# Kernel optimization log

Hardware: AMD Instinct MI355X
Metric: run time of the kernel (lower is better)

The kernel has to match this reference:

```python
import jax, jax.numpy as jnp
import numpy as np

N = 100000   # nodes
E = 1600000  # edges
NEG_SLOPE = 0.2
EPS = 1e-16


def _layer_norm(x, g, b):
    mu = jnp.mean(x, axis=-1, keepdims=True)
    var = jnp.mean((x - mu) ** 2, axis=-1, keepdims=True)
    return (x - mu) * jax.lax.rsqrt(var + 1e-5) * g + b


def _gat_layer(x, W, att_s, att_d, bias, src, dst, heads, C):
    n = x.shape[0]
    h = (x @ W.T).reshape(n, heads, C)            # [N,H,C]
    sa = jnp.sum(h * att_s, axis=-1)              # [N,H]
    da = jnp.sum(h * att_d, axis=-1)              # [N,H]
    logits = jax.nn.leaky_relu(sa[src] + da[dst], NEG_SLOPE)  # [E,H]
    m = jax.ops.segment_max(logits, dst, num_segments=n)      # [N,H]
    m = jnp.where(jnp.isfinite(m), m, 0.0)
    w = jnp.exp(logits - m[dst])                  # [E,H]
    denom = jax.ops.segment_sum(w, dst, num_segments=n)       # [N,H]
    msg = h[src] * w[:, :, None]                  # [E,H,C]
    agg = jax.ops.segment_sum(msg, dst, num_segments=n)       # [N,H,C]
    agg = agg / jnp.maximum(denom, EPS)[:, :, None]
    out = (agg + h).reshape(n, heads * C) + bias  # residual + bias
    return out


def setup_inputs() -> dict:
    key = jax.random.key(0)
    ks = jax.random.split(key, 16)
    s = 0.05
    inp = {
        "x": jax.random.normal(ks[0], (N, 128), jnp.float32),
        "edge_src": jax.random.randint(ks[1], (E,), 0, N, jnp.int32),
        "edge_dst": jax.random.randint(ks[2], (E,), 0, N, jnp.int32),
        # layer 1: in 128 -> heads=2, C=32 (out width 64)
        "W1": jax.random.normal(ks[3], (64, 128), jnp.float32) * s,
        "as1": jax.random.normal(ks[4], (2, 32), jnp.float32) * s,
        "ad1": jax.random.normal(ks[5], (2, 32), jnp.float32) * s,
        "b1": jnp.zeros((64,), jnp.float32),
        # layer 2: 64 -> heads=2, C=32
        "W2": jax.random.normal(ks[6], (64, 64), jnp.float32) * s,
        "as2": jax.random.normal(ks[7], (2, 32), jnp.float32) * s,
        "ad2": jax.random.normal(ks[8], (2, 32), jnp.float32) * s,
        "b2": jnp.zeros((64,), jnp.float32),
        # layer 3 (last): 64 -> heads=1, C=32
        "W3": jax.random.normal(ks[9], (32, 64), jnp.float32) * s,
        "as3": jax.random.normal(ks[10], (1, 32), jnp.float32) * s,
        "ad3": jax.random.normal(ks[11], (1, 32), jnp.float32) * s,
        "b3": jnp.zeros((32,), jnp.float32),
        "gamma1": jnp.ones((64,), jnp.float32),
        "beta1": jnp.zeros((64,), jnp.float32),
        "gamma2": jnp.ones((64,), jnp.float32),
        "beta2": jnp.zeros((64,), jnp.float32),
    }
    return inp


def reference(x, edge_src, edge_dst, W1, as1, ad1, b1, W2, as2, ad2, b2,
              W3, as3, ad3, b3, gamma1, beta1, gamma2, beta2):
    h = _gat_layer(x, W1, as1, ad1, b1, edge_src, edge_dst, 2, 32)
    h = jax.nn.relu(_layer_norm(h, gamma1, beta1))
    h = _gat_layer(h, W2, as2, ad2, b2, edge_src, edge_dst, 2, 32)
    h = jax.nn.relu(_layer_norm(h, gamma2, beta2))
    h = _gat_layer(h, W3, as3, ad3, b3, edge_src, edge_dst, 1, 32)
    return h
```

## Files before the change

kernel.cpp:

```cpp
#include <hip/hip_runtime.h>
#include <hip/hip_fp16.h>

#define LEAKY 0.2f
#define BSH 7
#define BN 128
#define CHUNK 8192
#define NBMAX 1024

__device__ __forceinline__ float leaky(float l) {
  return l >= 0.f ? l : LEAKY * l;
}

typedef _Float16 f16x2 __attribute__((ext_vector_type(2)));

__device__ __forceinline__ float fdot2(unsigned a, unsigned b, float c) {
#if __has_builtin(__builtin_amdgcn_fdot2)
  return __builtin_amdgcn_fdot2(__builtin_bit_cast(f16x2, a),
                                __builtin_bit_cast(f16x2, b), c, false);
#else
  __half2 ha = *(__half2*)&a, hb = *(__half2*)&b;
  float2 fa = __half22float2(ha), fb = __half22float2(hb);
  return fmaf(fa.x, fb.x, fmaf(fa.y, fb.y, c));
#endif
}

__device__ __forceinline__ int packsplat(float w) {
  const __half2 s = __half2half2(__float2half(w));
  return *(const int*)&s;
}
__device__ __forceinline__ __half2 asH2(unsigned u) { return *(__half2*)&u; }

template<int K, int CO, int H, bool IN_F32>
__global__ __launch_bounds__(256, 6)
void gat_gemm3(const void* __restrict__ xin, const float* __restrict__ W,
               const float* __restrict__ atts, const float* __restrict__ attd,
               __half* __restrict__ hh, float* __restrict__ sa, float* __restrict__ da,
               int N) {
  constexpr int CG = CO / 4;
  constexpr int BM = (256 / CG) * 4;
  constexpr int BK = 64;
  constexpr int NK = K / BK;
  constexpr int C = CO / H;
  constexpr int LDW = BK / 2 + 4;

  __shared__ unsigned xs[BM][LDW];
  __shared__ unsigned ws[CO][LDW];

  const int t = (int)threadIdx.x;
  const int cg = t % CG;
  const int ng = t / CG;
  const int n0 = (int)blockIdx.x * BM;

  float acc[4][4] = {};

  for (int kb = 0; kb < NK; ++kb) {
    __syncthreads();
    if constexpr (IN_F32) {
      const float* x = (const float*)xin;
      constexpr int F4R = BK / 4;
      constexpr int TOT = BM * F4R;
      for (int f = t; f < TOT; f += 256) {
        const int r = f / F4R, c = f % F4R;
        int row = n0 + r; row = row < N ? row : N - 1;
        const float4 v = *(const float4*)(x + (size_t)row * K + kb * BK + c * 4);
        const __half2 h0 = __floats2half2_rn(v.x, v.y);
        const __half2 h1 = __floats2half2_rn(v.z, v.w);
        xs[r][c * 2]     = *(const unsigned*)&h0;
        xs[r][c * 2 + 1] = *(const unsigned*)&h1;
      }
    } else {
      const __half* x = (const __half*)xin;
      constexpr int U4R = BK / 8;
      constexpr int TOT = BM * U4R;
      for (int f = t; f < TOT; f += 256) {
        const int r = f / U4R, c = f % U4R;
        int row = n0 + r; row = row < N ? row : N - 1;
        const uint4 v = *(const uint4*)(x + (size_t)row * K + kb * BK + c * 8);
        *(uint4*)&xs[r][c * 4] = v;
      }
    }
    {
      constexpr int F4R = BK / 4;
      constexpr int TOT = CO * F4R;
      for (int f = t; f < TOT; f += 256) {
        const int r = f / F4R, c = f % F4R;
        const float4 v = *(const float4*)(W + (size_t)r * K + kb * BK + c * 4);
        const __half2 h0 = __floats2half2_rn(v.x, v.y);
        const __half2 h1 = __floats2half2_rn(v.z, v.w);
        ws[r][c * 2]     = *(const unsigned*)&h0;
        ws[r][c * 2 + 1] = *(const unsigned*)&h1;
      }
    }
    __syncthreads();
    #pragma unroll
    for (int k = 0; k < BK; k += 8) {
      uint4 xa[4], wb[4];
      #pragma unroll
      for (int i = 0; i < 4; ++i) xa[i] = *(const uint4*)&xs[ng * 4 + i][k / 2];
      #pragma unroll
      for (int j = 0; j < 4; ++j) wb[j] = *(const uint4*)&ws[cg + CG * j][k / 2];
      #pragma unroll
      for (int i = 0; i < 4; ++i) {
        #pragma unroll
        for (int j = 0; j < 4; ++j) {
          acc[i][j] = fdot2(xa[i].x, wb[j].x, acc[i][j]);
          acc[i][j] = fdot2(xa[i].y, wb[j].y, acc[i][j]);
          acc[i][j] = fdot2(xa[i].z, wb[j].z, acc[i][j]);
          acc[i][j] = fdot2(xa[i].w, wb[j].w, acc[i][j]);
        }
      }
    }
  }

  float as_[4], ad_[4];
  #pragma unroll
  for (int j = 0; j < 4; ++j) {
    as_[j] = atts[cg + CG * j];
    ad_[j] = attd[cg + CG * j];
  }
  float ps[4][H] = {}, pd[4][H] = {};
  #pragma unroll
  for (int i = 0; i < 4; ++i) {
    #pragma unroll
    for (int j = 0; j < 4; ++j) {
      const int hd = (CG * j) / C;
      ps[i][hd] = fmaf(acc[i][j], as_[j], ps[i][hd]);
      pd[i][hd] = fmaf(acc[i][j], ad_[j], pd[i][hd]);
    }
  }
  #pragma unroll
  for (int m = 1; m < CG; m <<= 1) {
    #pragma unroll
    for (int i = 0; i < 4; ++i) {
      #pragma unroll
      for (int hd = 0; hd < H; ++hd) {
        ps[i][hd] += __shfl_xor(ps[i][hd], m, 64);
        pd[i][hd] += __shfl_xor(pd[i][hd], m, 64);
      }
    }
  }

  #pragma unroll
  for (int i = 0; i < 4; ++i) {
    const int n = n0 + ng * 4 + i;
    if (n < N) {
      #pragma unroll
      for (int j = 0; j < 4; ++j)
        hh[(size_t)n * CO + cg + CG * j] = __float2half(acc[i][j]);
      if (cg == 0) {
        #pragma unroll
        for (int hd = 0; hd < H; ++hd) {
          sa[n * H + hd] = ps[i][hd];
          da[n * H + hd] = pd[i][hd];
        }
      }
    }
  }
}

__global__ __launch_bounds__(256)
void gat_edge2(const __half* __restrict__ hh,
               const float* __restrict__ sa, const float* __restrict__ da,
               const int* __restrict__ rowp, const int* __restrict__ col,
               const float* __restrict__ bias, const float* __restrict__ gamma,
               const float* __restrict__ beta, __half* __restrict__ out, int N) {
  __shared__ int2 wst[4][4][17][2];
  const int t = (int)threadIdx.x;
  const int lane = t & 63;
  const int wib = t >> 6;
  const int quarter = lane >> 4;
  const int l = lane & 15;
  const int headq = l >> 3;
  const int wgl = (int)((blockIdx.x * blockDim.x + t) >> 6);
  const int n = wgl * 4 + quarter;
  const bool valid = (n < N);
  const int nc = valid ? n : N - 1;
  const int beg = rowp[nc];
  const int end = rowp[nc + 1];
  const float2 dvv = *(const float2*)(da + (size_t)nc * 2);
  const __half2* __restrict__ hhp = (const __half2*)hh;

  const __half2 z = __float2half2_rn(0.f);
  __half2 aL0 = z, aH0 = z, aL1 = z, aH1 = z, aL2 = z, aH2 = z, aL3 = z, aH3 = z;
  __half2 q0 = z, q1 = z, q2 = z, q3 = z;

  for (int b0 = beg; b0 < end; b0 += 16) {
    const int cnt = min(16, end - b0);
    if (l < cnt) {
      const int s = col[b0 + l];
      const float2 p = *(const float2*)(sa + (size_t)s * 2);
      int2 e0; e0.x = s; e0.y = packsplat(__expf(leaky(p.x + dvv.x)));
      int2 e1; e1.x = s; e1.y = packsplat(__expf(leaky(p.y + dvv.y)));
      wst[wib][quarter][l][0] = e0;
      wst[wib][quarter][l][1] = e1;
    }
    int i = 0;
    for (; i + 4 <= cnt; i += 4) {
      const int2 e0 = wst[wib][quarter][i][headq];
      const int2 e1 = wst[wib][quarter][i + 1][headq];
      const int2 e2 = wst[wib][quarter][i + 2][headq];
      const int2 e3 = wst[wib][quarter][i + 3][headq];
      const uint2 h0 = *(const uint2*)(hhp + ((size_t)e0.x << 5) + 2 * l);
      const uint2 h1 = *(const uint2*)(hhp + ((size_t)e1.x << 5) + 2 * l);
      const uint2 h2 = *(const uint2*)(hhp + ((size_t)e2.x << 5) + 2 * l);
      const uint2 h3 = *(const uint2*)(hhp + ((size_t)e3.x << 5) + 2 * l);
      const __half2 w0 = asH2(e0.y), w1 = asH2(e1.y), w2 = asH2(e2.y), w3 = asH2(e3.y);
      q0 = __hadd2(q0, w0); q1 = __hadd2(q1, w1);
      q2 = __hadd2(q2, w2); q3 = __hadd2(q3, w3);
      aL0 = __hfma2(w0, asH2(h0.x), aL0); aH0 = __hfma2(w0, asH2(h0.y), aH0);
      aL1 = __hfma2(w1, asH2(h1.x), aL1); aH1 = __hfma2(w1, asH2(h1.y), aH1);
      aL2 = __hfma2(w2, asH2(h2.x), aL2); aH2 = __hfma2(w2, asH2(h2.y), aH2);
      aL3 = __hfma2(w3, asH2(h3.x), aL3); aH3 = __hfma2(w3, asH2(h3.y), aH3);
    }
    for (; i < cnt; ++i) {
      const int2 e = wst[wib][quarter][i][headq];
      const uint2 hv = *(const uint2*)(hhp + ((size_t)e.x << 5) + 2 * l);
      const __half2 w = asH2(e.y);
      q0 = __hadd2(q0, w);
      aL0 = __hfma2(w, asH2(hv.x), aL0);
      aH0 = __hfma2(w, asH2(hv.y), aH0);
    }
  }

  const float c0 = (__low2float(aL0) + __low2float(aL1)) + (__low2float(aL2) + __low2float(aL3));
  const float c1 = (__high2float(aL0) + __high2float(aL1)) + (__high2float(aL2) + __high2float(aL3));
  const float c2 = (__low2float(aH0) + __low2float(aH1)) + (__low2float(aH2) + __low2float(aH3));
  const float c3 = (__high2float(aH0) + __high2float(aH1)) + (__high2float(aH2) + __high2float(aH3));
  const float qf = (__low2float(q0) + __low2float(q1)) + (__low2float(q2) + __low2float(q3));

  const float inv = 1.f / fmaxf(qf, 1e-16f);
  const uint2 hr = *(const uint2*)(hhp + ((size_t)nc << 5) + 2 * l);
  const float2 r01 = __half22float2(asH2(hr.x));
  const float2 r23 = __half22float2(asH2(hr.y));
  const float4 bi = *(const float4*)(bias + 4 * l);
  float v0 = c0 * inv + r01.x + bi.x;
  float v1 = c1 * inv + r01.y + bi.y;
  float v2 = c2 * inv + r23.x + bi.z;
  float v3 = c3 * inv + r23.y + bi.w;
  {
    float s = (v0 + v1) + (v2 + v3);
    #pragma unroll
    for (int m = 1; m < 16; m <<= 1) s += __shfl_xor(s, m, 64);
    const float mu = s * (1.f / 64.f);
    const float d0 = v0 - mu, d1 = v1 - mu, d2 = v2 - mu, d3 = v3 - mu;
    float vs = (d0 * d0 + d1 * d1) + (d2 * d2 + d3 * d3);
    #pragma unroll
    for (int m = 1; m < 16; m <<= 1) vs += __shfl_xor(vs, m, 64);
    const float rs = rsqrtf(vs * (1.f / 64.f) + 1e-5f);
    const float4 g = *(const float4*)(gamma + 4 * l);
    const float4 be = *(const float4*)(beta + 4 * l);
    v0 = fmaxf(d0 * rs * g.x + be.x, 0.f);
    v1 = fmaxf(d1 * rs * g.y + be.y, 0.f);
    v2 = fmaxf(d2 * rs * g.z + be.z, 0.f);
    v3 = fmaxf(d3 * rs * g.w + be.w, 0.f);
  }
  if (valid) {
    const __half2 o01 = __floats2half2_rn(v0, v1);
    const __half2 o23 = __floats2half2_rn(v2, v3);
    uint2 o; o.x = *(const unsigned*)&o01; o.y = *(const unsigned*)&o23;
    *(uint2*)(out + (size_t)n * 64 + 4 * l) = o;
  }
}

__global__ __launch_bounds__(256)
void gat_edge1(const __half* __restrict__ hh,
               const float* __restrict__ sa, const float* __restrict__ da,
               const int* __restrict__ rowp, const int* __restrict__ col,
               const float* __restrict__ bias, float* __restrict__ out, int N) {
  __shared__ int2 wst[4][8][17];
  const int t = (int)threadIdx.x;
  const int lane = t & 63;
  const int wib = t >> 6;
  const int oct = lane >> 3;
  const int l = lane & 7;
  const int wgl = (int)((blockIdx.x * blockDim.x + t) >> 6);
  const int n = wgl * 8 + oct;
  const bool valid = (n < N);
  const int nc = valid ? n : N - 1;
  const int beg = rowp[nc];
  const int end = rowp[nc + 1];
  const float dv = da[nc];
  const __half2* __restrict__ hhp = (const __half2*)hh;

  const __half2 z = __float2half2_rn(0.f);
  __half2 aL0 = z, aH0 = z, aL1 = z, aH1 = z, aL2 = z, aH2 = z, aL3 = z, aH3 = z;
  __half2 q0 = z, q1 = z, q2 = z, q3 = z;

  for (int b0 = beg; b0 < end; b0 += 16) {
    const int cnt = min(16, end - b0);
    if (l < 8) {
      if (l < cnt) {
        const int s = col[b0 + l];
        int2 e; e.x = s; e.y = packsplat(__expf(leaky(sa[s] + dv)));
        wst[wib][oct][l] = e;
      }
      const int l8 = l + 8;
      if (l8 < cnt) {
        const int s = col[b0 + l8];
        int2 e; e.x = s; e.y = packsplat(__expf(leaky(sa[s] + dv)));
        wst[wib][oct][l8] = e;
      }
    }
    int i = 0;
    for (; i + 4 <= cnt; i += 4) {
      const int2 e0 = wst[wib][oct][i];
      const int2 e1 = wst[wib][oct][i + 1];
      const int2 e2 = wst[wib][oct][i + 2];
      const int2 e3 = wst[wib][oct][i + 3];
      const uint2 h0 = *(const uint2*)(hhp + ((size_t)e0.x << 4) + 2 * l);
      const uint2 h1 = *(const uint2*)(hhp + ((size_t)e1.x << 4) + 2 * l);
      const uint2 h2 = *(const uint2*)(hhp + ((size_t)e2.x << 4) + 2 * l);
      const uint2 h3 = *(const uint2*)(hhp + ((size_t)e3.x << 4) + 2 * l);
      const __half2 w0 = asH2(e0.y), w1 = asH2(e1.y), w2 = asH2(e2.y), w3 = asH2(e3.y);
      q0 = __hadd2(q0, w0); q1 = __hadd2(q1, w1);
      q2 = __hadd2(q2, w2); q3 = __hadd2(q3, w3);
      aL0 = __hfma2(w0, asH2(h0.x), aL0); aH0 = __hfma2(w0, asH2(h0.y), aH0);
      aL1 = __hfma2(w1, asH2(h1.x), aL1); aH1 = __hfma2(w1, asH2(h1.y), aH1);
      aL2 = __hfma2(w2, asH2(h2.x), aL2); aH2 = __hfma2(w2, asH2(h2.y), aH2);
      aL3 = __hfma2(w3, asH2(h3.x), aL3); aH3 = __hfma2(w3, asH2(h3.y), aH3);
    }
    for (; i < cnt; ++i) {
      const int2 e = wst[wib][oct][i];
      const uint2 hv = *(const uint2*)(hhp + ((size_t)e.x << 4) + 2 * l);
      const __half2 w = asH2(e.y);
      q0 = __hadd2(q0, w);
      aL0 = __hfma2(w, asH2(hv.x), aL0);
      aH0 = __hfma2(w, asH2(hv.y), aH0);
    }
  }

  const float c0 = (__low2float(aL0) + __low2float(aL1)) + (__low2float(aL2) + __low2float(aL3));
  const float c1 = (__high2float(aL0) + __high2float(aL1)) + (__high2float(aL2) + __high2float(aL3));
  const float c2 = (__low2float(aH0) + __low2float(aH1)) + (__low2float(aH2) + __low2float(aH3));
  const float c3 = (__high2float(aH0) + __high2float(aH1)) + (__high2float(aH2) + __high2float(aH3));
  const float qf = (__low2float(q0) + __low2float(q1)) + (__low2float(q2) + __low2float(q3));

  if (valid) {
    const float inv = 1.f / fmaxf(qf, 1e-16f);
    const uint2 hr = *(const uint2*)(hhp + ((size_t)nc << 4) + 2 * l);
    const float2 r01 = __half22float2(asH2(hr.x));
    const float2 r23 = __half22float2(asH2(hr.y));
    const float4 bi = *(const float4*)(bias + 4 * l);
    float4 o;
    o.x = c0 * inv + r01.x + bi.x;
    o.y = c1 * inv + r01.y + bi.y;
    o.z = c2 * inv + r23.x + bi.z;
    o.w = c3 * inv + r23.y + bi.w;
    *(float4*)(out + (size_t)n * 32 + 4 * l) = o;
  }
}

__global__ __launch_bounds__(256)
void k_hist_chunk(const int* __restrict__ dst, int* __restrict__ bcnt, int E, int NB) {
  __shared__ int lh[NBMAX];
  const int t = (int)threadIdx.x;
  const int c0 = (int)blockIdx.x * CHUNK;
  const int cnt = min(CHUNK, E - c0);
  for (int b = t; b < NB; b += 256) lh[b] = 0;
  __syncthreads();
  for (int i = t; i < cnt; i += 256)
    atomicAdd(&lh[dst[c0 + i] >> BSH], 1);
  __syncthreads();
  for (int b = t; b < NB; b += 256)
    if (lh[b]) atomicAdd(&bcnt[b], lh[b]);
}

__global__ void k_bscan(const int* __restrict__ bcnt, int nb,
                        int* __restrict__ bstart, int* __restrict__ bcur,
                        int* __restrict__ rowp_last, int E) {
  __shared__ int sm[256];
  const int t = (int)threadIdx.x;
  int v[4];
  #pragma unroll
  for (int j = 0; j < 4; ++j) { int i = t * 4 + j; v[j] = (i < nb) ? bcnt[i] : 0; }
  const int tot = v[0] + v[1] + v[2] + v[3];
  sm[t] = tot; __syncthreads();
  #pragma unroll
  for (int off = 1; off < 256; off <<= 1) {
    int xv = (t >= off) ? sm[t - off] : 0;
    __syncthreads();
    sm[t] += xv;
    __syncthreads();
  }
  int excl = sm[t] - tot;
  #pragma unroll
  for (int j = 0; j < 4; ++j) {
    int i = t * 4 + j;
    if (i < nb) { bstart[i] = excl; bcur[i] = excl; excl += v[j]; }
  }
  if (t == 0) { bstart[nb] = E; *rowp_last = E; }
}

__global__ __launch_bounds__(256)
void k_part(const int* __restrict__ src, const int* __restrict__ dst,
            int* __restrict__ bcur, int* __restrict__ pairs, int E, int NB) {
  __shared__ int lh[NBMAX];
  __shared__ int lofs[NBMAX];
  __shared__ int gofs[NBMAX];
  __shared__ int stg[CHUNK];
  __shared__ short stgb[CHUNK];
  __shared__ int bsum[256];
  const int t = (int)threadIdx.x;
  const int c0 = (int)blockIdx.x * CHUNK;
  const int cnt = min(CHUNK, E - c0);

  for (int b = t; b < NB; b += 256) lh[b] = 0;
  __syncthreads();
  for (int i = t; i < cnt; i += 256)
    atomicAdd(&lh[dst[c0 + i] >> BSH], 1);
  __syncthreads();

  int v[4]; int run = 0;
  #pragma unroll
  for (int j = 0; j < 4; ++j) {
    const int b = t * 4 + j;
    v[j] = (b < NB) ? lh[b] : 0;
    run += v[j];
  }
  bsum[t] = run;
  __syncthreads();
  #pragma unroll
  for (int off = 1; off < 256; off <<= 1) {
    int xv = (t >= off) ? bsum[t - off] : 0;
    __syncthreads();
    bsum[t] += xv;
    __syncthreads();
  }
  int base = bsum[t] - run;
  #pragma unroll
  for (int j = 0; j < 4; ++j) {
    const int b = t * 4 + j;
    if (b < NB) lofs[b] = base;
    base += v[j];
  }
  __syncthreads();

  for (int b = t; b < NB; b += 256) {
    const int c = lh[b];
    gofs[b] = c ? atomicAdd(&bcur[b], c) : 0;
    lh[b] = lofs[b];
  }
  __syncthreads();

  for (int i = t; i < cnt; i += 256) {
    const int d = dst[c0 + i];
    const int b = d >> BSH;
    const int p = atomicAdd(&lh[b], 1);
    stg[p] = (src[c0 + i] << BSH) | (d & (BN - 1));
    stgb[p] = (short)b;
  }
  __syncthreads();

  for (int i = t; i < cnt; i += 256) {
    const int b = (int)stgb[i];
    pairs[gofs[b] + (i - lofs[b])] = stg[i];
  }
}

__global__ __launch_bounds__(256)
void k_bucket_csr(const int* __restrict__ pairs, const int* __restrict__ bstart,
                  int* __restrict__ rowp, int* __restrict__ col, int N) {
  __shared__ int ldeg[BN];
  __shared__ int lofs[BN];
  const int b = (int)blockIdx.x;
  const int t = (int)threadIdx.x;
  const int base = b << BSH;
  const int nn = min(BN, N - base);
  const int s0 = bstart[b];
  const int s1 = bstart[b + 1];

  if (t < BN) ldeg[t] = 0;
  __syncthreads();
  for (int i = s0 + t; i < s1; i += 256)
    atomicAdd(&ldeg[pairs[i] & (BN - 1)], 1);
  __syncthreads();
  if (t < BN) lofs[t] = ldeg[t];
  __syncthreads();
  #pragma unroll
  for (int off = 1; off < BN; off <<= 1) {
    int v = (t < BN && t >= off) ? lofs[t - off] : 0;
    __syncthreads();
    if (t < BN) lofs[t] += v;
    __syncthreads();
  }
  if (t < BN) {
    const int ofs = s0 + lofs[t] - ldeg[t];
    if (t < nn) rowp[base + t] = ofs;
    ldeg[t] = ofs;
  }
  __syncthreads();
  for (int i = s0 + t; i < s1; i += 256) {
    const int pr = pairs[i];
    const int p = atomicAdd(&ldeg[pr & (BN - 1)], 1);
    col[p] = pr >> BSH;
  }
}

extern "C" void kernel_launch(void* const* d_in, const int* in_sizes, int n_in,
                              void* d_out, int out_size, void* d_ws, size_t ws_size,
                              hipStream_t stream) {
  const float* x   = (const float*)d_in[0];
  const int* esrc  = (const int*)d_in[1];
  const int* edst  = (const int*)d_in[2];
  const float* W1  = (const float*)d_in[3];
  const float* as1 = (const float*)d_in[4];
  const float* ad1 = (const float*)d_in[5];
  const float* b1  = (const float*)d_in[6];
  const float* W2  = (const float*)d_in[7];
  const float* as2 = (const float*)d_in[8];
  const float* ad2 = (const float*)d_in[9];
  const float* b2  = (const float*)d_in[10];
  const float* W3  = (const float*)d_in[11];
  const float* as3 = (const float*)d_in[12];
  const float* ad3 = (const float*)d_in[13];
  const float* b3  = (const float*)d_in[14];
  const float* g1  = (const float*)d_in[15];
  const float* be1 = (const float*)d_in[16];
  const float* g2  = (const float*)d_in[17];
  const float* be2 = (const float*)d_in[18];

  const int N = in_sizes[0] / 128;
  const int E = in_sizes[1];
  const int NB = (N + BN - 1) / BN;

  char* ws = (char*)d_ws;
  size_t off = 0;
  auto alloc = [&](size_t bytes) -> void* {
    void* p = ws + off;
    off = (off + bytes + 255) & ~(size_t)255;
    return p;
  };
  __half* lnbuf = (__half*)alloc((size_t)N * 64 * 2);
  __half* hh   = (__half*)alloc((size_t)N * 64 * 2);
  float* sab   = (float*)alloc((size_t)N * 2 * 4);
  float* dab   = (float*)alloc((size_t)N * 2 * 4);
  int* rowp    = (int*)alloc((size_t)(N + 1) * 4);
  int* colb    = (int*)alloc((size_t)E * 4);
  int* bcnt    = (int*)alloc((size_t)NB * 4);
  int* bstart  = (int*)alloc((size_t)(NB + 1) * 4);
  int* bcur    = (int*)alloc((size_t)NB * 4);
  int* pairs = (E <= out_size) ? (int*)d_out : (int*)alloc((size_t)E * 4);
  (void)ws_size; (void)n_in;

  hipMemsetAsync(bcnt, 0, (size_t)NB * 4, stream);
  const int NW = (E + CHUNK - 1) / CHUNK;
  k_hist_chunk<<<NW, 256, 0, stream>>>(edst, bcnt, E, NB);
  k_bscan<<<1, 256, 0, stream>>>(bcnt, NB, bstart, bcur, rowp + N, E);
  k_part<<<NW, 256, 0, stream>>>(esrc, edst, bcur, pairs, E, NB);
  k_bucket_csr<<<NB, 256, 0, stream>>>(pairs, bstart, rowp, colb, N);

  const int gG12 = (N + 63) / 64;
  const int gG3  = (N + 127) / 128;
  const int gE2 = (N + 15) / 16;
  const int gE1 = (N + 31) / 32;

  gat_gemm3<128, 64, 2, true><<<gG12, 256, 0, stream>>>(x, W1, as1, ad1, hh, sab, dab, N);
  gat_edge2<<<gE2, 256, 0, stream>>>(hh, sab, dab, rowp, colb, b1, g1, be1, lnbuf, N);

  gat_gemm3<64, 64, 2, false><<<gG12, 256, 0, stream>>>(lnbuf, W2, as2, ad2, hh, sab, dab, N);
  gat_edge2<<<gE2, 256, 0, stream>>>(hh, sab, dab, rowp, colb, b2, g2, be2, lnbuf, N);

  gat_gemm3<64, 32, 1, false><<<gG3, 256, 0, stream>>>(lnbuf, W3, as3, ad3, hh, sab, dab, N);
  gat_edge1<<<gE1, 256, 0, stream>>>(hh, sab, dab, rowp, colb, b3, (float*)d_out, N);
}
```

Baseline: 235.1 us.

## Prefetch next edge batch, unroll gather by 8, deterministic chunk-offset partition

```diff
diff --git a/kernel.cpp b/kernel.cpp
--- a/kernel.cpp
+++ b/kernel.cpp
@@ -4,7 +4,7 @@
 #define LEAKY 0.2f
 #define BSH 7
 #define BN 128
-#define CHUNK 8192
+#define CHUNK 4096
 #define NBMAX 1024
 
 __device__ __forceinline__ float leaky(float l) {
@@ -182,35 +182,70 @@
 
   const __half2 z = __float2half2_rn(0.f);
   __half2 aL0 = z, aH0 = z, aL1 = z, aH1 = z, aL2 = z, aH2 = z, aL3 = z, aH3 = z;
-  __half2 q0 = z, q1 = z, q2 = z, q3 = z;
+  __half2 q0 = z, q1 = z;
+
+  int sP = 0; float2 pP = make_float2(0.f, 0.f);
+  if (beg < end) {
+    const int cnt0 = min(16, end - beg);
+    if (l < cnt0) {
+      sP = col[beg + l];
+      pP = *(const float2*)(sa + (size_t)sP * 2);
+    }
+  }
 
   for (int b0 = beg; b0 < end; b0 += 16) {
     const int cnt = min(16, end - b0);
     if (l < cnt) {
-      const int s = col[b0 + l];
-      const float2 p = *(const float2*)(sa + (size_t)s * 2);
-      int2 e0; e0.x = s; e0.y = packsplat(__expf(leaky(p.x + dvv.x)));
-      int2 e1; e1.x = s; e1.y = packsplat(__expf(leaky(p.y + dvv.y)));
+      int2 e0; e0.x = sP; e0.y = packsplat(__expf(leaky(pP.x + dvv.x)));
+      int2 e1; e1.x = sP; e1.y = packsplat(__expf(leaky(pP.y + dvv.y)));
       wst[wib][quarter][l][0] = e0;
       wst[wib][quarter][l][1] = e1;
     }
+    const int nb0 = b0 + 16;
+    if (nb0 < end) {
+      const int ncnt = min(16, end - nb0);
+      if (l < ncnt) {
+        sP = col[nb0 + l];
+        pP = *(const float2*)(sa + (size_t)sP * 2);
+      }
+    }
     int i = 0;
+    for (; i + 8 <= cnt; i += 8) {
+      int2 e[8];
+      #pragma unroll
+      for (int j = 0; j < 8; ++j) e[j] = wst[wib][quarter][i + j][headq];
+      uint2 hv[8];
+      #pragma unroll
+      for (int j = 0; j < 8; ++j) hv[j] = *(const uint2*)(hhp + ((size_t)e[j].x << 5) + 2 * l);
+      __half2 w[8];
+      #pragma unroll
+      for (int j = 0; j < 8; ++j) w[j] = asH2(e[j].y);
+      q0 = __hadd2(q0, __hadd2(__hadd2(w[0], w[1]), __hadd2(w[2], w[3])));
+      q1 = __hadd2(q1, __hadd2(__hadd2(w[4], w[5]), __hadd2(w[6], w[7])));
+      aL0 = __hfma2(w[0], asH2(hv[0].x), aL0); aH0 = __hfma2(w[0], asH2(hv[0].y), aH0);
+      aL1 = __hfma2(w[1], asH2(hv[1].x), aL1); aH1 = __hfma2(w[1], asH2(hv[1].y), aH1);
+      aL2 = __hfma2(w[2], asH2(hv[2].x), aL2); aH2 = __hfma2(w[2], asH2(hv[2].y), aH2);
+      aL3 = __hfma2(w[3], asH2(hv[3].x), aL3); aH3 = __hfma2(w[3], asH2(hv[3].y), aH3);
+      aL0 = __hfma2(w[4], asH2(hv[4].x), aL0); aH0 = __hfma2(w[4], asH2(hv[4].y), aH0);
+      aL1 = __hfma2(w[5], asH2(hv[5].x), aL1); aH1 = __hfma2(w[5], asH2(hv[5].y), aH1);
+      aL2 = __hfma2(w[6], asH2(hv[6].x), aL2); aH2 = __hfma2(w[6], asH2(hv[6].y), aH2);
+      aL3 = __hfma2(w[7], asH2(hv[7].x), aL3); aH3 = __hfma2(w[7], asH2(hv[7].y), aH3);
+    }
     for (; i + 4 <= cnt; i += 4) {
-      const int2 e0 = wst[wib][quarter][i][headq];
-      const int2 e1 = wst[wib][quarter][i + 1][headq];
-      const int2 e2 = wst[wib][quarter][i + 2][headq];
-      const int2 e3 = wst[wib][quarter][i + 3][headq];
-      const uint2 h0 = *(const uint2*)(hhp + ((size_t)e0.x << 5) + 2 * l);
-      const uint2 h1 = *(const uint2*)(hhp + ((size_t)e1.x << 5) + 2 * l);
-      const uint2 h2 = *(const uint2*)(hhp + ((size_t)e2.x << 5) + 2 * l);
-      const uint2 h3 = *(const uint2*)(hhp + ((size_t)e3.x << 5) + 2 * l);
-      const __half2 w0 = asH2(e0.y), w1 = asH2(e1.y), w2 = asH2(e2.y), w3 = asH2(e3.y);
-      q0 = __hadd2(q0, w0); q1 = __hadd2(q1, w1);
-      q2 = __hadd2(q2, w2); q3 = __hadd2(q3, w3);
-      aL0 = __hfma2(w0, asH2(h0.x), aL0); aH0 = __hfma2(w0, asH2(h0.y), aH0);
-      aL1 = __hfma2(w1, asH2(h1.x), aL1); aH1 = __hfma2(w1, asH2(h1.y), aH1);
-      aL2 = __hfma2(w2, asH2(h2.x), aL2); aH2 = __hfma2(w2, asH2(h2.y), aH2);
-      aL3 = __hfma2(w3, asH2(h3.x), aL3); aH3 = __hfma2(w3, asH2(h3.y), aH3);
+      int2 e[4];
+      #pragma unroll
+      for (int j = 0; j < 4; ++j) e[j] = wst[wib][quarter][i + j][headq];
+      uint2 hv[4];
+      #pragma unroll
+      for (int j = 0; j < 4; ++j) hv[j] = *(const uint2*)(hhp + ((size_t)e[j].x << 5) + 2 * l);
+      __half2 w[4];
+      #pragma unroll
+      for (int j = 0; j < 4; ++j) w[j] = asH2(e[j].y);
+      q0 = __hadd2(q0, __hadd2(__hadd2(w[0], w[1]), __hadd2(w[2], w[3])));
+      aL0 = __hfma2(w[0], asH2(hv[0].x), aL0); aH0 = __hfma2(w[0], asH2(hv[0].y), aH0);
+      aL1 = __hfma2(w[1], asH2(hv[1].x), aL1); aH1 = __hfma2(w[1], asH2(hv[1].y), aH1);
+      aL2 = __hfma2(w[2], asH2(hv[2].x), aL2); aH2 = __hfma2(w[2], asH2(hv[2].y), aH2);
+      aL3 = __hfma2(w[3], asH2(hv[3].x), aL3); aH3 = __hfma2(w[3], asH2(hv[3].y), aH3);
     }
     for (; i < cnt; ++i) {
       const int2 e = wst[wib][quarter][i][headq];
@@ -226,7 +261,7 @@
   const float c1 = (__high2float(aL0) + __high2float(aL1)) + (__high2float(aL2) + __high2float(aL3));
   const float c2 = (__low2float(aH0) + __low2float(aH1)) + (__low2float(aH2) + __low2float(aH3));
   const float c3 = (__high2float(aH0) + __high2float(aH1)) + (__high2float(aH2) + __high2float(aH3));
-  const float qf = (__low2float(q0) + __low2float(q1)) + (__low2float(q2) + __low2float(q3));
+  const float qf = __low2float(q0) + __low2float(q1);
 
   const float inv = 1.f / fmaxf(qf, 1e-16f);
   const uint2 hr = *(const uint2*)(hhp + ((size_t)nc << 5) + 2 * l);
@@ -267,7 +302,7 @@
                const float* __restrict__ sa, const float* __restrict__ da,
                const int* __restrict__ rowp, const int* __restrict__ col,
                const float* __restrict__ bias, float* __restrict__ out, int N) {
-  __shared__ int2 wst[4][8][17];
+  __shared__ int2 wst[4][8][9];
   const int t = (int)threadIdx.x;
   const int lane = t & 63;
   const int wib = t >> 6;
@@ -284,40 +319,62 @@
 
   const __half2 z = __float2half2_rn(0.f);
   __half2 aL0 = z, aH0 = z, aL1 = z, aH1 = z, aL2 = z, aH2 = z, aL3 = z, aH3 = z;
-  __half2 q0 = z, q1 = z, q2 = z, q3 = z;
-
-  for (int b0 = beg; b0 < end; b0 += 16) {
-    const int cnt = min(16, end - b0);
-    if (l < 8) {
-      if (l < cnt) {
-        const int s = col[b0 + l];
-        int2 e; e.x = s; e.y = packsplat(__expf(leaky(sa[s] + dv)));
-        wst[wib][oct][l] = e;
-      }
-      const int l8 = l + 8;
-      if (l8 < cnt) {
-        const int s = col[b0 + l8];
-        int2 e; e.x = s; e.y = packsplat(__expf(leaky(sa[s] + dv)));
-        wst[wib][oct][l8] = e;
-      }
+  __half2 q0 = z, q1 = z;
+
+  int sP = 0; float pP = 0.f;
+  if (beg < end) {
+    const int cnt0 = min(8, end - beg);
+    if (l < cnt0) { sP = col[beg + l]; pP = sa[sP]; }
+  }
+
+  for (int b0 = beg; b0 < end; b0 += 8) {
+    const int cnt = min(8, end - b0);
+    if (l < cnt) {
+      int2 e; e.x = sP; e.y = packsplat(__expf(leaky(pP + dv)));
+      wst[wib][oct][l] = e;
+    }
+    const int nb0 = b0 + 8;
+    if (nb0 < end) {
+      const int ncnt = min(8, end - nb0);
+      if (l < ncnt) { sP = col[nb0 + l]; pP = sa[sP]; }
     }
     int i = 0;
+    for (; i + 8 <= cnt; i += 8) {
+      int2 e[8];
+      #pragma unroll
+      for (int j = 0; j < 8; ++j) e[j] = wst[wib][oct][i + j];
+      uint2 hv[8];
+      #pragma unroll
+      for (int j = 0; j < 8; ++j) hv[j] = *(const uint2*)(hhp + ((size_t)e[j].x << 4) + 2 * l);
+      __half2 w[8];
+      #pragma unroll
+      for (int j = 0; j < 8; ++j) w[j] = asH2(e[j].y);
+      q0 = __hadd2(q0, __hadd2(__hadd2(w[0], w[1]), __hadd2(w[2], w[3])));
+      q1 = __hadd2(q1, __hadd2(__hadd2(w[4], w[5]), __hadd2(w[6], w[7])));
+      aL0 = __hfma2(w[0], asH2(hv[0].x), aL0); aH0 = __hfma2(w[0], asH2(hv[0].y), aH0);
+      aL1 = __hfma2(w[1], asH2(hv[1].x), aL1); aH1 = __hfma2(w[1], asH2(hv[1].y), aH1);
+      aL2 = __hfma2(w[2], asH2(hv[2].x), aL2); aH2 = __hfma2(w[2], asH2(hv[2].y), aH2);
+      aL3 = __hfma2(w[3], asH2(hv[3].x), aL3); aH3 = __hfma2(w[3], asH2(hv[3].y), aH3);
+      aL0 = __hfma2(w[4], asH2(hv[4].x), aL0); aH0 = __hfma2(w[4], asH2(hv[4].y), aH0);
+      aL1 = __hfma2(w[5], asH2(hv[5].x), aL1); aH1 = __hfma2(w[5], asH2(hv[5].y), aH1);
+      aL2 = __hfma2(w[6], asH2(hv[6].x), aL2); aH2 = __hfma2(w[6], asH2(hv[6].y), aH2);
+      aL3 = __hfma2(w[7], asH2(hv[7].x), aL3); aH3 = __hfma2(w[7], asH2(hv[7].y), aH3);
+    }
     for (; i + 4 <= cnt; i += 4) {
-      const int2 e0 = wst[wib][oct][i];
-      const int2 e1 = wst[wib][oct][i + 1];
-      const int2 e2 = wst[wib][oct][i + 2];
-      const int2 e3 = wst[wib][oct][i + 3];
-      const uint2 h0 = *(const uint2*)(hhp + ((size_t)e0.x << 4) + 2 * l);
-      const uint2 h1 = *(const uint2*)(hhp + ((size_t)e1.x << 4) + 2 * l);
-      const uint2 h2 = *(const uint2*)(hhp + ((size_t)e2.x << 4) + 2 * l);
-      const uint2 h3 = *(const uint2*)(hhp + ((size_t)e3.x << 4) + 2 * l);
-      const __half2 w0 = asH2(e0.y), w1 = asH2(e1.y), w2 = asH2(e2.y), w3 = asH2(e3.y);
-      q0 = __hadd2(q0, w0); q1 = __hadd2(q1, w1);
-      q2 = __hadd2(q2, w2); q3 = __hadd2(q3, w3);
-      aL0 = __hfma2(w0, asH2(h0.x), aL0); aH0 = __hfma2(w0, asH2(h0.y), aH0);
-      aL1 = __hfma2(w1, asH2(h1.x), aL1); aH1 = __hfma2(w1, asH2(h1.y), aH1);
-      aL2 = __hfma2(w2, asH2(h2.x), aL2); aH2 = __hfma2(w2, asH2(h2.y), aH2);
-      aL3 = __hfma2(w3, asH2(h3.x), aL3); aH3 = __hfma2(w3, asH2(h3.y), aH3);
+      int2 e[4];
+      #pragma unroll
+      for (int j = 0; j < 4; ++j) e[j] = wst[wib][oct][i + j];
+      uint2 hv[4];
+      #pragma unroll
+      for (int j = 0; j < 4; ++j) hv[j] = *(const uint2*)(hhp + ((size_t)e[j].x << 4) + 2 * l);
+      __half2 w[4];
+      #pragma unroll
+      for (int j = 0; j < 4; ++j) w[j] = asH2(e[j].y);
+      q0 = __hadd2(q0, __hadd2(__hadd2(w[0], w[1]), __hadd2(w[2], w[3])));
+      aL0 = __hfma2(w[0], asH2(hv[0].x), aL0); aH0 = __hfma2(w[0], asH2(hv[0].y), aH0);
+      aL1 = __hfma2(w[1], asH2(hv[1].x), aL1); aH1 = __hfma2(w[1], asH2(hv[1].y), aH1);
+      aL2 = __hfma2(w[2], asH2(hv[2].x), aL2); aH2 = __hfma2(w[2], asH2(hv[2].y), aH2);
+      aL3 = __hfma2(w[3], asH2(hv[3].x), aL3); aH3 = __hfma2(w[3], asH2(hv[3].y), aH3);
     }
     for (; i < cnt; ++i) {
       const int2 e = wst[wib][oct][i];
@@ -333,7 +390,7 @@
   const float c1 = (__high2float(aL0) + __high2float(aL1)) + (__high2float(aL2) + __high2float(aL3));
   const float c2 = (__low2float(aH0) + __low2float(aH1)) + (__low2float(aH2) + __low2float(aH3));
   const float c3 = (__high2float(aH0) + __high2float(aH1)) + (__high2float(aH2) + __high2float(aH3));
-  const float qf = (__low2float(q0) + __low2float(q1)) + (__low2float(q2) + __low2float(q3));
+  const float qf = __low2float(q0) + __low2float(q1);
 
   if (valid) {
     const float inv = 1.f / fmaxf(qf, 1e-16f);
@@ -350,24 +407,40 @@
   }
 }
 
+
 __global__ __launch_bounds__(256)
-void k_hist_chunk(const int* __restrict__ dst, int* __restrict__ bcnt, int E, int NB) {
+void k_hist_chunk(const int* __restrict__ dst, int* __restrict__ cntmat,
+                  int E, int NB) {
   __shared__ int lh[NBMAX];
   const int t = (int)threadIdx.x;
-  const int c0 = (int)blockIdx.x * CHUNK;
+  const int chunk = (int)blockIdx.x;
+  const int c0 = chunk * CHUNK;
   const int cnt = min(CHUNK, E - c0);
   for (int b = t; b < NB; b += 256) lh[b] = 0;
   __syncthreads();
   for (int i = t; i < cnt; i += 256)
     atomicAdd(&lh[dst[c0 + i] >> BSH], 1);
   __syncthreads();
-  for (int b = t; b < NB; b += 256)
-    if (lh[b]) atomicAdd(&bcnt[b], lh[b]);
+  int* row = cntmat + (size_t)chunk * NB;
+  for (int b = t; b < NB; b += 256) row[b] = lh[b];
+}
+
+__global__ void k_colscan(int* __restrict__ cntmat, int* __restrict__ bcnt,
+                          int NB, int NW) {
+  const int b = (int)(blockIdx.x * blockDim.x + threadIdx.x);
+  if (b >= NB) return;
+  int run = 0;
+  for (int c = 0; c < NW; ++c) {
+    const size_t idx = (size_t)c * NB + b;
+    const int v = cntmat[idx];
+    cntmat[idx] = run;
+    run += v;
+  }
+  bcnt[b] = run;
 }
 
 __global__ void k_bscan(const int* __restrict__ bcnt, int nb,
-                        int* __restrict__ bstart, int* __restrict__ bcur,
-                        int* __restrict__ rowp_last, int E) {
+                        int* __restrict__ bstart, int* __restrict__ rowp_last, int E) {
   __shared__ int sm[256];
   const int t = (int)threadIdx.x;
   int v[4];
@@ -386,14 +459,15 @@
   #pragma unroll
   for (int j = 0; j < 4; ++j) {
     int i = t * 4 + j;
-    if (i < nb) { bstart[i] = excl; bcur[i] = excl; excl += v[j]; }
+    if (i < nb) { bstart[i] = excl; excl += v[j]; }
   }
   if (t == 0) { bstart[nb] = E; *rowp_last = E; }
 }
 
 __global__ __launch_bounds__(256)
 void k_part(const int* __restrict__ src, const int* __restrict__ dst,
-            int* __restrict__ bcur, int* __restrict__ pairs, int E, int NB) {
+            const int* __restrict__ bstart, const int* __restrict__ cntmat,
+            int* __restrict__ pairs, int E, int NB) {
   __shared__ int lh[NBMAX];
   __shared__ int lofs[NBMAX];
   __shared__ int gofs[NBMAX];
@@ -401,7 +475,8 @@
   __shared__ short stgb[CHUNK];
   __shared__ int bsum[256];
   const int t = (int)threadIdx.x;
-  const int c0 = (int)blockIdx.x * CHUNK;
+  const int chunk = (int)blockIdx.x;
+  const int c0 = chunk * CHUNK;
   const int cnt = min(CHUNK, E - c0);
 
   for (int b = t; b < NB; b += 256) lh[b] = 0;
@@ -435,9 +510,9 @@
   }
   __syncthreads();
 
+  const int* crow = cntmat + (size_t)chunk * NB;
   for (int b = t; b < NB; b += 256) {
-    const int c = lh[b];
-    gofs[b] = c ? atomicAdd(&bcur[b], c) : 0;
+    gofs[b] = bstart[b] + crow[b];
     lh[b] = lofs[b];
   }
   __syncthreads();
@@ -522,6 +597,7 @@
   const int N = in_sizes[0] / 128;
   const int E = in_sizes[1];
   const int NB = (N + BN - 1) / BN;
+  const int NW = (E + CHUNK - 1) / CHUNK;
 
   char* ws = (char*)d_ws;
   size_t off = 0;
@@ -538,15 +614,14 @@
   int* colb    = (int*)alloc((size_t)E * 4);
   int* bcnt    = (int*)alloc((size_t)NB * 4);
   int* bstart  = (int*)alloc((size_t)(NB + 1) * 4);
-  int* bcur    = (int*)alloc((size_t)NB * 4);
+  int* cntmat  = (int*)alloc((size_t)NW * NB * 4);
   int* pairs = (E <= out_size) ? (int*)d_out : (int*)alloc((size_t)E * 4);
   (void)ws_size; (void)n_in;
 
-  hipMemsetAsync(bcnt, 0, (size_t)NB * 4, stream);
-  const int NW = (E + CHUNK - 1) / CHUNK;
-  k_hist_chunk<<<NW, 256, 0, stream>>>(edst, bcnt, E, NB);
-  k_bscan<<<1, 256, 0, stream>>>(bcnt, NB, bstart, bcur, rowp + N, E);
-  k_part<<<NW, 256, 0, stream>>>(esrc, edst, bcur, pairs, E, NB);
+  k_hist_chunk<<<NW, 256, 0, stream>>>(edst, cntmat, E, NB);
+  k_colscan<<<(NB + 255) / 256, 256, 0, stream>>>(cntmat, bcnt, NB, NW);
+  k_bscan<<<1, 256, 0, stream>>>(bcnt, NB, bstart, rowp + N, E);
+  k_part<<<NW, 256, 0, stream>>>(esrc, edst, bstart, cntmat, pairs, E, NB);
   k_bucket_csr<<<NB, 256, 0, stream>>>(pairs, bstart, rowp, colb, N);
 
   const int gG12 = (N + 63) / 64;
```

Result: slower. 305.3 us (+29.8%).
